# Optimization experiments

Measured on AMD Instinct MI355X. Metric: run time of the kernel, lower is better.

The kernel has to match this reference:

```python
import jax, jax.numpy as jnp
import numpy as np

B, T, D, E = 4, 2048, 1024, 8


def setup_inputs() -> dict:
    key = jax.random.key(0)
    ks = jax.random.split(key, 8)
    scale_g = float(np.sqrt(2.0 / (D + E)))  # xavier_uniform-ish scale for W_g
    scale_w = float(1.0 / np.sqrt(D))
    return {
        "x": jax.random.normal(ks[0], (B, T, D), dtype=jnp.float32),
        "noise": jax.random.normal(ks[1], (B, T, E), dtype=jnp.float32),  # the N(0,1) sample in Gating.forward
        "W_g": jax.random.normal(ks[2], (D, E), dtype=jnp.float32) * scale_g,
        "W_noise": jax.random.normal(ks[3], (D, E), dtype=jnp.float32),
        "W1": jax.random.normal(ks[4], (E, D, D), dtype=jnp.float32) * scale_w,
        "b1": jnp.zeros((E, D), dtype=jnp.float32),
        "W2": jax.random.normal(ks[5], (E, D, D), dtype=jnp.float32) * scale_w,
        "b2": jnp.zeros((E, D), dtype=jnp.float32),
        "k": 2,
    }


def _gates(x, noise, W_g, W_noise, k):
    # h = x@W_g + N(0,1) + softplus(x@W_noise)   (note: noise added, not scaled)
    h = jnp.einsum("btd,de->bte", x, W_g) + noise + jax.nn.softplus(
        jnp.einsum("btd,de->bte", x, W_noise)
    )
    kth = jax.lax.top_k(h, k)[0][..., -1:]           # kth largest per token
    h_masked = jnp.where(h >= kth, h, -jnp.inf)       # keepTopK (ties kept, as in torch)
    return jax.nn.softmax(h_masked, axis=-1)          # [B,T,E]


def reference(x, noise, W_g, W_noise, W1, b1, W2, b2, k):
    gates = _gates(x, noise, W_g, W_noise, k)
    # Dense loop over experts (faithful to original): every expert FFN on all tokens.
    # hidden: [E,B,T,D]
    hidden = jax.nn.relu(jnp.einsum("btd,edh->ebth", x, W1) + b1[:, None, None, :])
    expert_out = jnp.einsum("ebth,eho->ebto", hidden, W2) + b2[:, None, None, :]
    # mask-weighted combine: sum_e expert_out_e * gates[...,e]
    return jnp.einsum("ebtd,bte->btd", expert_out, gates)
```

## Files before the change

kernel.cpp:

```cpp
#include <hip/hip_runtime.h>
#include <hip/hip_bf16.h>

#define BTOK 8192
#define DDIM 1024
#define NEXP 8

typedef unsigned short u16;
typedef unsigned int u32;
typedef __attribute__((ext_vector_type(8))) short short8;
typedef __attribute__((ext_vector_type(4))) float f32x4;

constexpr int BM = 128, BN = 128, BK = 64;
constexpr int SLOTCAP = 3072;
constexpr int NT = DDIM / BK;

__device__ __forceinline__ u16 f2bf(float f){
  __hip_bfloat16 h = __float2bfloat16(f);
  return *reinterpret_cast<u16*>(&h);
}
__device__ __forceinline__ float bf2f(u16 v){
  return __uint_as_float(((u32)v) << 16);
}
__device__ __forceinline__ void gll16(const u16* gsrc, u16* ldst){
  __builtin_amdgcn_global_load_lds((const __attribute__((address_space(1))) void*)gsrc,
                                   (__attribute__((address_space(3))) void*)ldst,
                                   16, 0, 0);
}

#define GTOK 16
__global__ __launch_bounds__(512) void gating_score_kernel(
    const float* __restrict__ x, const float* __restrict__ noise,
    const float* __restrict__ Wg, const float* __restrict__ Wn,
    float* __restrict__ h_out, u16* __restrict__ xb)
{
  __shared__ float lw[2][NEXP][4][260];
  const int tid = threadIdx.x;

  for (int i = tid; i < 2*DDIM*NEXP; i += 512){
    const int mat = i >> 13;
    const int r   = i & 8191;
    const int d = r >> 3, ee = r & 7;
    const float* W = mat ? Wn : Wg;
    lw[mat][ee][d >> 8][d & 255] = W[r];
  }
  __syncthreads();

  const int q   = tid & 3;
  const int e   = (tid >> 2) & 7;
  const int tok = tid >> 5;
  const int t   = blockIdx.x * GTOK + tok;

  const float4* x4 = reinterpret_cast<const float4*>(x + (size_t)t*DDIM + q*256);
  const float4* g4 = reinterpret_cast<const float4*>(&lw[0][e][q][0]);
  const float4* n4 = reinterpret_cast<const float4*>(&lw[1][e][q][0]);
  ushort4* xb4 = reinterpret_cast<ushort4*>(xb + (size_t)t*DDIM + q*256);
  float agx=0.f, agz=0.f, anx=0.f, anz=0.f;
  #pragma unroll 8
  for (int j = 0; j < 64; ++j){
    const float4 xv = x4[j];
    const float4 wg = g4[j];
    const float4 wn = n4[j];
    agx = fmaf(xv.x,wg.x, fmaf(xv.y,wg.y, agx));
    agz = fmaf(xv.z,wg.z, fmaf(xv.w,wg.w, agz));
    anx = fmaf(xv.x,wn.x, fmaf(xv.y,wn.y, anx));
    anz = fmaf(xv.z,wn.z, fmaf(xv.w,wn.w, anz));
    if (e == 0)
      xb4[j] = make_ushort4(f2bf(xv.x), f2bf(xv.y), f2bf(xv.z), f2bf(xv.w));
  }
  float ag = agx + agz, an = anx + anz;
  ag += __shfl_xor(ag, 1); an += __shfl_xor(an, 1);
  ag += __shfl_xor(ag, 2); an += __shfl_xor(an, 2);
  if (q == 0){
    const float sp = (an > 20.f) ? an : log1pf(expf(an));
    h_out[(size_t)t*NEXP + e] = ag + noise[(size_t)t*NEXP + e] + sp;
  }
}

__global__ __launch_bounds__(256) void gating_select_kernel(
    const float* __restrict__ h_in, const int* __restrict__ kp,
    float* __restrict__ gates, int* __restrict__ counts, int* __restrict__ lists,
    int* __restrict__ tokmap, int* __restrict__ ncnt)
{
  __shared__ int lcnt[NEXP];
  __shared__ int lbase[NEXP];
  const int tid = threadIdx.x;
  const int t   = blockIdx.x*256 + tid;
  if (tid < NEXP) lcnt[tid] = 0;
  __syncthreads();

  float h[NEXP];
  const float4 h0 = reinterpret_cast<const float4*>(h_in + (size_t)t*NEXP)[0];
  const float4 h1 = reinterpret_cast<const float4*>(h_in + (size_t)t*NEXP)[1];
  h[0]=h0.x; h[1]=h0.y; h[2]=h0.z; h[3]=h0.w;
  h[4]=h1.x; h[5]=h1.y; h[6]=h1.z; h[7]=h1.w;

  int kk = *kp; kk = kk<1?1:(kk>NEXP?NEXP:kk);
  bool used[NEXP];
  #pragma unroll
  for (int e=0;e<NEXP;e++) used[e]=false;
  float kth = 0.f;
  for (int i=0;i<kk;i++){
    int bi=0; float bv=-3.4e38f;
    #pragma unroll
    for (int e=0;e<NEXP;e++) if (!used[e] && h[e]>bv){bv=h[e]; bi=e;}
    used[bi]=true; kth=bv;
  }
  float m=-3.4e38f;
  #pragma unroll
  for (int e=0;e<NEXP;e++) if (h[e]>=kth && h[e]>m) m=h[e];
  float p[NEXP], s=0.f;
  #pragma unroll
  for (int e=0;e<NEXP;e++){ p[e]=(h[e]>=kth)?expf(h[e]-m):0.f; s+=p[e]; }
  const float inv = 1.f/s;
  float g[NEXP];
  int lslot[NEXP];
  #pragma unroll
  for (int e=0;e<NEXP;e++){
    g[e] = p[e]*inv;
    gates[(size_t)t*NEXP + e] = g[e];
    if (g[e] > 0.f) lslot[e] = atomicAdd(&lcnt[e], 1);
  }
  __syncthreads();
  if (tid < NEXP) lbase[tid] = atomicAdd(&counts[tid], lcnt[tid]);
  __syncthreads();
  int idx = 0;
  #pragma unroll
  for (int e=0;e<NEXP;e++){
    if (g[e] > 0.f){
      const int slot = lbase[e] + lslot[e];
      lists[e*BTOK + slot] = t;
      tokmap[t*NEXP + idx] = (e << 13) | (slot & 8191);
      idx++;
    }
  }
  ncnt[t] = idx;
}

__global__ __launch_bounds__(256) void trans_kernel(
    const float* __restrict__ W1, const float* __restrict__ W2,
    u16* __restrict__ W1T, u16* __restrict__ W2T)
{
  __shared__ float tile[64][65];
  const int mz = blockIdx.z;
  const float* src = (mz < NEXP) ? (W1  + (size_t)mz*DDIM*DDIM) : (W2  + (size_t)(mz-NEXP)*DDIM*DDIM);
  u16*       dst = (mz < NEXP) ? (W1T + (size_t)mz*DDIM*DDIM) : (W2T + (size_t)(mz-NEXP)*DDIM*DDIM);
  const int r0 = blockIdx.x*64, c0 = blockIdx.y*64;
  const int tx = threadIdx.x & 63, ty = threadIdx.x >> 6;
  #pragma unroll
  for (int i=ty;i<64;i+=4)
    tile[i][tx] = src[(size_t)(r0+i)*DDIM + c0+tx];
  __syncthreads();
  #pragma unroll
  for (int i=ty;i<64;i+=4)
    dst[(size_t)(c0+i)*DDIM + r0+tx] = f2bf(tile[tx][i]);
}

template<int LAYER>
__device__ __forceinline__ void ffn_body(
    const u16* __restrict__ Asrc, const u16* __restrict__ WT,
    const float* __restrict__ bias,
    const int* __restrict__ counts, const int* __restrict__ lists,
    u16* __restrict__ dst)
{
  const int e  = blockIdx.z;
  int cnt = counts[e]; if (cnt > SLOTCAP) cnt = SLOTCAP;
  const int m0 = blockIdx.x*BM;
  if (m0 >= cnt) return;
  const int n0 = blockIdx.y*BN;

  __shared__ __align__(16) u16 ldsA[2][BM*BK];
  __shared__ __align__(16) u16 ldsB[2][BN*BK];

  const int tid = threadIdx.x;
  const int wave = tid>>6, lane = tid&63;
  const int wm = wave>>1, wn = wave&1;

  const u16* aSrc[4]; const u16* bSrc[4];
  {
    const int lr = lane>>3, sp = lane&7;
    #pragma unroll
    for (int i=0;i<4;i++){
      const int row = wave*32 + i*8 + lr;
      const int ku  = sp ^ (row&7);
      size_t abase;
      if constexpr (LAYER==1){
        int gr = m0 + row; if (gr >= cnt) gr = cnt-1;
        const int tok = lists[e*BTOK + gr];
        abase = (size_t)tok * DDIM;
      } else {
        abase = ((size_t)e*SLOTCAP + m0 + row) * DDIM;
      }
      aSrc[i] = Asrc + abase + ku*8;
      bSrc[i] = WT + ((size_t)e*DDIM + n0 + row)*DDIM + ku*8;
    }
  }

  const int q = lane>>4, l16 = lane&15;
  int aoff[2][4], boff[2][4];
  #pragma unroll
  for (int f=0;f<4;f++){
    const int ra = wm*64 + f*16 + l16;
    const int rb = wn*64 + f*16 + l16;
    #pragma unroll
    for (int kk=0;kk<2;kk++){
      aoff[kk][f] = ra*BK + (((kk*4+q) ^ (ra&7))*8);
      boff[kk][f] = rb*BK + (((kk*4+q) ^ (rb&7))*8);
    }
  }

  f32x4 acc[4][4];
  #pragma unroll
  for (int i=0;i<4;i++)
    #pragma unroll
    for (int j=0;j<4;j++)
      acc[i][j] = (f32x4){0.f,0.f,0.f,0.f};

  #pragma unroll
  for (int i=0;i<4;i++){
    gll16(aSrc[i], &ldsA[0][(wave*4+i)*512]);
    gll16(bSrc[i], &ldsB[0][(wave*4+i)*512]);
  }
  __syncthreads();

  int cur = 0;
  for (int kt = 0; kt < NT-1; ++kt){
    #pragma unroll
    for (int i=0;i<4;i++){
      gll16(aSrc[i] + (size_t)(kt+1)*BK, &ldsA[cur^1][(wave*4+i)*512]);
      gll16(bSrc[i] + (size_t)(kt+1)*BK, &ldsB[cur^1][(wave*4+i)*512]);
    }
    #pragma unroll
    for (int kk=0;kk<2;kk++){
      short8 af[4], bfv[4];
      #pragma unroll
      for (int f=0;f<4;f++) af[f]  = *reinterpret_cast<const short8*>(&ldsA[cur][aoff[kk][f]]);
      #pragma unroll
      for (int f=0;f<4;f++) bfv[f] = *reinterpret_cast<const short8*>(&ldsB[cur][boff[kk][f]]);
      #pragma unroll
      for (int fm=0;fm<4;fm++)
        #pragma unroll
        for (int fn=0;fn<4;fn++)
          acc[fm][fn] = __builtin_amdgcn_mfma_f32_16x16x32_bf16(af[fm], bfv[fn], acc[fm][fn], 0, 0, 0);
    }
    __syncthreads();
    cur ^= 1;
  }
  #pragma unroll
  for (int kk=0;kk<2;kk++){
    short8 af[4], bfv[4];
    #pragma unroll
    for (int f=0;f<4;f++) af[f]  = *reinterpret_cast<const short8*>(&ldsA[cur][aoff[kk][f]]);
    #pragma unroll
    for (int f=0;f<4;f++) bfv[f] = *reinterpret_cast<const short8*>(&ldsB[cur][boff[kk][f]]);
    #pragma unroll
    for (int fm=0;fm<4;fm++)
      #pragma unroll
      for (int fn=0;fn<4;fn++)
        acc[fm][fn] = __builtin_amdgcn_mfma_f32_16x16x32_bf16(af[fm], bfv[fn], acc[fm][fn], 0, 0, 0);
  }

  #pragma unroll
  for (int fm=0;fm<4;fm++){
    #pragma unroll
    for (int r=0;r<4;r++){
      const int row = wm*64 + fm*16 + q*4 + r;
      const int gr  = m0 + row;
      #pragma unroll
      for (int fn=0;fn<4;fn++){
        const int col = n0 + wn*64 + fn*16 + l16;
        float v = acc[fm][fn][r] + bias[e*DDIM + col];
        if constexpr (LAYER==1) v = v > 0.f ? v : 0.f;
        dst[((size_t)e*SLOTCAP + gr)*DDIM + col] = f2bf(v);
      }
    }
  }
}

__global__ __launch_bounds__(256) void ffn1_kernel(
    const u16* __restrict__ A, const u16* __restrict__ WT, const float* __restrict__ b,
    const int* __restrict__ counts, const int* __restrict__ lists, u16* __restrict__ dst)
{ ffn_body<1>(A, WT, b, counts, lists, dst); }

__global__ __launch_bounds__(256) void ffn2_kernel(
    const u16* __restrict__ A, const u16* __restrict__ WT, const float* __restrict__ b,
    const int* __restrict__ counts, const int* __restrict__ lists, u16* __restrict__ dst)
{ ffn_body<2>(A, WT, b, counts, lists, dst); }

__global__ __launch_bounds__(256) void combine_kernel(
    const u16* __restrict__ partial, const int* __restrict__ tokmap,
    const int* __restrict__ ncnt, const float* __restrict__ gates,
    float* __restrict__ out)
{
  const int t = blockIdx.x, c = threadIdx.x;
  const int n = ncnt[t];
  float4 acc = {0.f, 0.f, 0.f, 0.f};
  for (int j = 0; j < n; ++j){
    const int ent  = tokmap[t*NEXP + j];
    const int e    = ent >> 13, slot = ent & 8191;
    if (slot >= SLOTCAP) continue;
    const float g = gates[(size_t)t*NEXP + e];
    const ushort4 pv = reinterpret_cast<const ushort4*>(
        partial + ((size_t)e*SLOTCAP + slot)*DDIM)[c];
    acc.x = fmaf(g, bf2f(pv.x), acc.x);
    acc.y = fmaf(g, bf2f(pv.y), acc.y);
    acc.z = fmaf(g, bf2f(pv.z), acc.z);
    acc.w = fmaf(g, bf2f(pv.w), acc.w);
  }
  reinterpret_cast<float4*>(out + (size_t)t*DDIM)[c] = acc;
}

extern "C" void kernel_launch(void* const* d_in, const int* in_sizes, int n_in,
                              void* d_out, int out_size, void* d_ws, size_t ws_size,
                              hipStream_t stream)
{
  const float* x     = (const float*)d_in[0];
  const float* noise = (const float*)d_in[1];
  const float* Wg    = (const float*)d_in[2];
  const float* Wn    = (const float*)d_in[3];
  const float* W1    = (const float*)d_in[4];
  const float* b1    = (const float*)d_in[5];
  const float* W2    = (const float*)d_in[6];
  const float* b2    = (const float*)d_in[7];
  const int*   kp    = (const int*)d_in[8];
  float* out = (float*)d_out;

  char* ws = (char*)d_ws;
  int*   counts = (int*)ws;
  int*   lists  = (int*)(ws + 4096);
  float* gates  = (float*)(ws + 266240);
  int*   tokmap = (int*)(ws + 528384);
  int*   ncnt   = (int*)(ws + 790528);
  float* hbuf   = (float*)(ws + 823296);
  u16*   xb     = (u16*)(ws + 1085440);
  u16*   W1T    = (u16*)(ws + 17862656);
  u16*   W2T    = (u16*)(ws + 34639872);
  u16*   hidden = (u16*)(ws + 51417088);
  u16*   partial= (u16*)(ws + 101748736);
  const size_t NEED = 152080384ull;

  hipMemsetAsync(counts, 0, 64, stream);
  if (ws_size < NEED){
    hipMemsetAsync(d_out, 0, (size_t)out_size*sizeof(float), stream);
    return;
  }

  trans_kernel<<<dim3(16,16,16), 256, 0, stream>>>(W1, W2, W1T, W2T);
  gating_score_kernel<<<BTOK/GTOK, 512, 0, stream>>>(x, noise, Wg, Wn, hbuf, xb);
  gating_select_kernel<<<BTOK/256, 256, 0, stream>>>(hbuf, kp, gates, counts, lists,
                                                     tokmap, ncnt);
  ffn1_kernel<<<dim3(SLOTCAP/BM, DDIM/BN, NEXP), 256, 0, stream>>>(
      xb, W1T, b1, counts, lists, hidden);
  ffn2_kernel<<<dim3(SLOTCAP/BM, DDIM/BN, NEXP), 256, 0, stream>>>(
      hidden, W2T, b2, counts, lists, partial);
  combine_kernel<<<BTOK, 256, 0, stream>>>(partial, tokmap, ncnt, gates, out);
}
```

Measured before the change: 330.5 us.

## Enlarge expert GEMM tiles to 256x256 with 8 waves and explicit double-buffer pipeline

The expert FFN GEMMs move from 128x128 tiles with 4 waves to 256x256 tiles with 8 waves (512 threads), each wave computing 128x64 of output. This raises data reuse per loaded byte and halves the grid in each dimension. The main loop is rewritten with two stages prefetched up front, explicit vmcnt waits and raw s_barriers, plus s_setprio around the MFMA bursts to overlap loads with compute. The larger tiles use 128 KB of LDS per block and more accumulator registers, and with the 3072-slot capacity there are fewer blocks to spread across CUs.

```diff
diff --git a/kernel.cpp b/kernel.cpp
--- a/kernel.cpp
+++ b/kernel.cpp
@@ -10,7 +10,7 @@
 typedef __attribute__((ext_vector_type(8))) short short8;
 typedef __attribute__((ext_vector_type(4))) float f32x4;
 
-constexpr int BM = 128, BN = 128, BK = 64;
+constexpr int BM = 256, BN = 256, BK = 64;
 constexpr int SLOTCAP = 3072;
 constexpr int NT = DDIM / BK;
 
@@ -173,7 +173,7 @@
 
   const int tid = threadIdx.x;
   const int wave = tid>>6, lane = tid&63;
-  const int wm = wave>>1, wn = wave&1;
+  const int wm = wave>>2, wn = wave&3;
 
   const u16* aSrc[4]; const u16* bSrc[4];
   {
@@ -185,8 +185,7 @@
       size_t abase;
       if constexpr (LAYER==1){
         int gr = m0 + row; if (gr >= cnt) gr = cnt-1;
-        const int tok = lists[e*BTOK + gr];
-        abase = (size_t)tok * DDIM;
+        abase = (size_t)lists[e*BTOK + gr] * DDIM;
       } else {
         abase = ((size_t)e*SLOTCAP + m0 + row) * DDIM;
       }
@@ -196,74 +195,77 @@
   }
 
   const int q = lane>>4, l16 = lane&15;
-  int aoff[2][4], boff[2][4];
+  int aoff[8], boff[4];
+  #pragma unroll
+  for (int f=0;f<8;f++){
+    const int ra = wm*128 + f*16 + l16;
+    aoff[f] = ra*BK + ((q ^ (ra&7))*8);
+  }
   #pragma unroll
   for (int f=0;f<4;f++){
-    const int ra = wm*64 + f*16 + l16;
     const int rb = wn*64 + f*16 + l16;
-    #pragma unroll
-    for (int kk=0;kk<2;kk++){
-      aoff[kk][f] = ra*BK + (((kk*4+q) ^ (ra&7))*8);
-      boff[kk][f] = rb*BK + (((kk*4+q) ^ (rb&7))*8);
-    }
-  }
-
-  f32x4 acc[4][4];
-  #pragma unroll
-  for (int i=0;i<4;i++)
+    boff[f] = rb*BK + ((q ^ (rb&7))*8);
+  }
+
+  f32x4 acc[8][4];
+  #pragma unroll
+  for (int i=0;i<8;i++)
     #pragma unroll
     for (int j=0;j<4;j++)
       acc[i][j] = (f32x4){0.f,0.f,0.f,0.f};
 
-  #pragma unroll
-  for (int i=0;i<4;i++){
-    gll16(aSrc[i], &ldsA[0][(wave*4+i)*512]);
-    gll16(bSrc[i], &ldsB[0][(wave*4+i)*512]);
-  }
-  __syncthreads();
-
-  int cur = 0;
-  for (int kt = 0; kt < NT-1; ++kt){
-    #pragma unroll
-    for (int i=0;i<4;i++){
-      gll16(aSrc[i] + (size_t)(kt+1)*BK, &ldsA[cur^1][(wave*4+i)*512]);
-      gll16(bSrc[i] + (size_t)(kt+1)*BK, &ldsB[cur^1][(wave*4+i)*512]);
-    }
-    #pragma unroll
-    for (int kk=0;kk<2;kk++){
-      short8 af[4], bfv[4];
+  #define STAGE(T, c)                                            \
+    _Pragma("unroll")                                            \
+    for (int i=0;i<4;i++){                                       \
+      gll16(aSrc[i] + (size_t)(T)*BK, &ldsA[c][(wave*32+i*8)*BK]); \
+      gll16(bSrc[i] + (size_t)(T)*BK, &ldsB[c][(wave*32+i*8)*BK]); \
+    }
+
+  STAGE(0, 0)
+  STAGE(1, 1)
+  asm volatile("s_waitcnt vmcnt(8)" ::: "memory");
+  __builtin_amdgcn_sched_barrier(0);
+  __builtin_amdgcn_s_barrier();
+  __builtin_amdgcn_sched_barrier(0);
+
+  for (int kt = 0; kt < NT; ++kt){
+    const int c = kt & 1;
+    #pragma unroll
+    for (int kk=0; kk<2; kk++){
+      const int kx = kk ? 32 : 0;
+      short8 bfr[4], afr[8];
       #pragma unroll
-      for (int f=0;f<4;f++) af[f]  = *reinterpret_cast<const short8*>(&ldsA[cur][aoff[kk][f]]);
+      for (int f=0;f<4;f++) bfr[f] = *reinterpret_cast<const short8*>(&ldsB[c][boff[f] ^ kx]);
       #pragma unroll
-      for (int f=0;f<4;f++) bfv[f] = *reinterpret_cast<const short8*>(&ldsB[cur][boff[kk][f]]);
+      for (int f=0;f<8;f++) afr[f] = *reinterpret_cast<const short8*>(&ldsA[c][aoff[f] ^ kx]);
+      __builtin_amdgcn_s_setprio(1);
       #pragma unroll
-      for (int fm=0;fm<4;fm++)
+      for (int fm=0;fm<8;fm++)
         #pragma unroll
         for (int fn=0;fn<4;fn++)
-          acc[fm][fn] = __builtin_amdgcn_mfma_f32_16x16x32_bf16(af[fm], bfv[fn], acc[fm][fn], 0, 0, 0);
-    }
-    __syncthreads();
-    cur ^= 1;
-  }
-  #pragma unroll
-  for (int kk=0;kk<2;kk++){
-    short8 af[4], bfv[4];
-    #pragma unroll
-    for (int f=0;f<4;f++) af[f]  = *reinterpret_cast<const short8*>(&ldsA[cur][aoff[kk][f]]);
-    #pragma unroll
-    for (int f=0;f<4;f++) bfv[f] = *reinterpret_cast<const short8*>(&ldsB[cur][boff[kk][f]]);
-    #pragma unroll
-    for (int fm=0;fm<4;fm++)
-      #pragma unroll
-      for (int fn=0;fn<4;fn++)
-        acc[fm][fn] = __builtin_amdgcn_mfma_f32_16x16x32_bf16(af[fm], bfv[fn], acc[fm][fn], 0, 0, 0);
-  }
-
-  #pragma unroll
-  for (int fm=0;fm<4;fm++){
+          acc[fm][fn] = __builtin_amdgcn_mfma_f32_16x16x32_bf16(afr[fm], bfr[fn], acc[fm][fn], 0, 0, 0);
+      __builtin_amdgcn_s_setprio(0);
+    }
+    __builtin_amdgcn_sched_barrier(0);
+    __builtin_amdgcn_s_barrier();
+    __builtin_amdgcn_sched_barrier(0);
+    if (kt + 2 < NT){
+      STAGE(kt+2, c)
+      asm volatile("s_waitcnt vmcnt(8)" ::: "memory");
+    } else {
+      asm volatile("s_waitcnt vmcnt(0)" ::: "memory");
+    }
+    __builtin_amdgcn_sched_barrier(0);
+    __builtin_amdgcn_s_barrier();
+    __builtin_amdgcn_sched_barrier(0);
+  }
+  #undef STAGE
+
+  #pragma unroll
+  for (int fm=0;fm<8;fm++){
     #pragma unroll
     for (int r=0;r<4;r++){
-      const int row = wm*64 + fm*16 + q*4 + r;
+      const int row = wm*128 + fm*16 + q*4 + r;
       const int gr  = m0 + row;
       #pragma unroll
       for (int fn=0;fn<4;fn++){
@@ -276,12 +278,12 @@
   }
 }
 
-__global__ __launch_bounds__(256) void ffn1_kernel(
+__global__ __launch_bounds__(512, 2) void ffn1_kernel(
     const u16* __restrict__ A, const u16* __restrict__ WT, const float* __restrict__ b,
     const int* __restrict__ counts, const int* __restrict__ lists, u16* __restrict__ dst)
 { ffn_body<1>(A, WT, b, counts, lists, dst); }
 
-__global__ __launch_bounds__(256) void ffn2_kernel(
+__global__ __launch_bounds__(512, 2) void ffn2_kernel(
     const u16* __restrict__ A, const u16* __restrict__ WT, const float* __restrict__ b,
     const int* __restrict__ counts, const int* __restrict__ lists, u16* __restrict__ dst)
 { ffn_body<2>(A, WT, b, counts, lists, dst); }
@@ -348,9 +350,9 @@
   gating_score_kernel<<<BTOK/GTOK, 512, 0, stream>>>(x, noise, Wg, Wn, hbuf, xb);
   gating_select_kernel<<<BTOK/256, 256, 0, stream>>>(hbuf, kp, gates, counts, lists,
                                                      tokmap, ncnt);
-  ffn1_kernel<<<dim3(SLOTCAP/BM, DDIM/BN, NEXP), 256, 0, stream>>>(
+  ffn1_kernel<<<dim3(SLOTCAP/BM, DDIM/BN, NEXP), 512, 0, stream>>>(
       xb, W1T, b1, counts, lists, hidden);
-  ffn2_kernel<<<dim3(SLOTCAP/BM, DDIM/BN, NEXP), 256, 0, stream>>>(
+  ffn2_kernel<<<dim3(SLOTCAP/BM, DDIM/BN, NEXP), 512, 0, stream>>>(
       hidden, W2T, b2, counts, lists, partial);
   combine_kernel<<<BTOK, 256, 0, stream>>>(partial, tokmap, ncnt, gates, out);
 }
```

Measured after the change: 349.1 us. +5.6%, slower.
